# Kernel optimization log

Hardware: AMD Instinct MI355X
Metric: run time of the kernel (lower is better)

Reference implementation:

```python
import jax, jax.numpy as jnp
import numpy as np

ALPHA = 0.1  # LeakyReLU slope

def _leaky(v):
    return jnp.where(v >= 0, v, ALPHA * v)

def setup_inputs() -> dict:
    key = jax.random.key(0)
    k1, k2, k3 = jax.random.split(key, 3)
    B, D_IN, D1, D2 = 262144, 200, 150, 100
    x = jax.random.normal(k1, (B, D_IN), dtype=jnp.float32)
    W1 = jax.random.normal(k2, (D_IN, D1), dtype=jnp.float32) * 0.05
    b1 = jnp.zeros((D1,), dtype=jnp.float32)
    W2 = jax.random.normal(k3, (D1, D2), dtype=jnp.float32) * 0.05
    b2 = jnp.zeros((D2,), dtype=jnp.float32)
    return {"x": x, "W1": W1, "b1": b1, "W2": W2, "b2": b2}

def reference(x, W1, b1, W2, b2):
    # Original loops per sample: dense(200->150)+LeakyReLU, mean -> out1;
    # dense(150->100)+LeakyReLU, mean -> out2. Batched here as single GEMMs.
    h1 = _leaky(x @ W1 + b1)           # [B, 150]
    out1 = jnp.mean(h1, axis=-1)       # [B]
    h2 = _leaky(h1 @ W2 + b2)          # [B, 100]
    out2 = jnp.mean(h2, axis=-1)       # [B]
    return (out1, out2)
```

## Files before the change

### kernel.cpp

```cpp
#include <hip/hip_runtime.h>

typedef unsigned short u16;
typedef unsigned int u32;
typedef __bf16 bf16x8 __attribute__((ext_vector_type(8)));
typedef float f32x4 __attribute__((ext_vector_type(4)));

#define W2F_OFF 71680
#define B1_OFF 107520
#define B2_OFF 108160
#define WS_BYTES 108608

__device__ __align__(256) unsigned char g_wbuf[WS_BYTES];

__device__ __forceinline__ u16 f2bf(float f) {
  __bf16 b = (__bf16)f;
  return __builtin_bit_cast(u16, b);
}
__device__ __forceinline__ u32 pk2bf(float a, float b) {
  return (u32)f2bf(a) | ((u32)f2bf(b) << 16);
}

__global__ void prep_kernel(const float* __restrict__ W1, const float* __restrict__ b1,
                            const float* __restrict__ W2, const float* __restrict__ b2)
{
  const int stride = gridDim.x * blockDim.x;
  const int tid0 = blockIdx.x * blockDim.x + threadIdx.x;
  u16* w1f = (u16*)g_wbuf;
  for (int e = tid0; e < 35840; e += stride) {
    int j = e & 7, l = (e >> 3) & 63, nt = (e >> 9) % 10, kt = e / 5120;
    int k = kt * 32 + ((l >> 4) << 3) + j;
    int n = nt * 16 + (l & 15);
    w1f[e] = (k < 200 && n < 150) ? f2bf(W1[k * 150 + n]) : (u16)0;
  }
  u16* w2f = (u16*)(g_wbuf + W2F_OFF);
  for (int e = tid0; e < 17920; e += stride) {
    int j = e & 7, l = (e >> 3) & 63, nt = (e >> 9) % 7, kt = e / 3584;
    int k = kt * 32 + ((l >> 4) << 3) + j;
    int n = nt * 16 + (l & 15);
    w2f[e] = (k < 150 && n < 100) ? f2bf(W2[k * 100 + n]) : (u16)0;
  }
  float* b1p = (float*)(g_wbuf + B1_OFF);
  for (int e = tid0; e < 160; e += stride) b1p[e] = (e < 150) ? b1[e] : 0.f;
  float* b2p = (float*)(g_wbuf + B2_OFF);
  for (int e = tid0; e < 112; e += stride) b2p[e] = (e < 100) ? b2[e] : 0.f;
}

__global__ __launch_bounds__(512, 5)
void fused_mlp(const float* __restrict__ x, float* __restrict__ out, int B)
{
  __shared__ __align__(16) u16 xs[12800];
  __shared__ float ps[2][2][64];

  const int tid = threadIdx.x;
  const int lane = tid & 63;
  const int wv = tid >> 6;
  const int h = wv & 1;
  const int mt = wv >> 1;
  const int cl = lane & 15, gr = lane >> 4;
  const long r0 = (long)blockIdx.x * 64;

  const u16* w1g = (const u16*)g_wbuf;
  const u16* w2g = (const u16*)(g_wbuf + W2F_OFF);

  const float* xg = x + r0 * 200;
  #pragma unroll
  for (int i = 0; i < 7; ++i) {
    int c = tid + i * 512;
    if (c < 3200) {
      int row = c / 50, kc = c % 50;
      float4 v = *reinterpret_cast<const float4*>(xg + row * 200 + kc * 4);
      int k0 = kc * 4;
      int m = row >> 4;
      int idx;
      if (k0 < 192) {
        int F = m * 6 + (k0 >> 5);
        int fl = (row & 15) | (((k0 & 31) >> 3) << 4);
        idx = (F * 64 + (fl ^ (F & 7))) * 8 + (k0 & 7);
      } else {
        idx = 12288 + m * 128 + (row & 15) * 8 + (k0 - 192);
      }
      uint2 p;
      p.x = pk2bf(v.x, v.y);
      p.y = pk2bf(v.z, v.w);
      *reinterpret_cast<uint2*>(&xs[idx]) = p;
    }
  }

  bf16x8 bfr[5];
  #pragma unroll
  for (int nt = 0; nt < 5; ++nt)
    bfr[nt] = *reinterpret_cast<const bf16x8*>(w1g + ((0 * 10 + 5 * h + nt) * 64 + lane) * 8);

  __syncthreads();

  const f32x4 zz = {0.f, 0.f, 0.f, 0.f};
  f32x4 acc1[5];
  #pragma unroll
  for (int nt = 0; nt < 5; ++nt) acc1[nt] = zz;

  #pragma unroll
  for (int kt = 0; kt < 7; ++kt) {
    bf16x8 bnx[5];
    if (kt < 6) {
      #pragma unroll
      for (int nt = 0; nt < 5; ++nt)
        bnx[nt] = *reinterpret_cast<const bf16x8*>(w1g + (((kt + 1) * 10 + 5 * h + nt) * 64 + lane) * 8);
    }
    bf16x8 a;
    if (kt < 6) {
      int F = mt * 6 + kt;
      a = *reinterpret_cast<const bf16x8*>(&xs[(F * 64 + (lane ^ (F & 7))) * 8]);
    } else {
      union { bf16x8 v; u32 w[4]; } A;
      A.v = *reinterpret_cast<const bf16x8*>(&xs[12288 + mt * 128 + cl * 8]);
      if (gr != 0) { A.w[0] = A.w[1] = A.w[2] = A.w[3] = 0u; }
      a = A.v;
    }
    #pragma unroll
    for (int nt = 0; nt < 5; ++nt)
      acc1[nt] = __builtin_amdgcn_mfma_f32_16x16x32_bf16(a, bfr[nt], acc1[nt], 0, 0, 0);
    if (kt < 6) {
      #pragma unroll
      for (int nt = 0; nt < 5; ++nt) bfr[nt] = bnx[nt];
    }
  }
  __syncthreads();

  const float* b1p = (const float*)(g_wbuf + B1_OFF);
  float b1v[5];
  #pragma unroll
  for (int nt = 0; nt < 5; ++nt) b1v[nt] = b1p[(5 * h + nt) * 16 + cl];

  float rs[4] = {0, 0, 0, 0};
  #pragma unroll
  for (int nt = 0; nt < 5; ++nt) {
    int k2 = (5 * h + nt) * 16 + cl;
    int kt2 = k2 >> 5;
    int l2base = 16 * ((k2 & 31) >> 3);
    int e2 = k2 & 7;
    #pragma unroll
    for (int j = 0; j < 4; ++j) {
      int l2 = gr * 4 + j + l2base;
      float hv = acc1[nt][j] + b1v[nt];
      hv = (hv >= 0.f) ? hv : 0.1f * hv;
      rs[j] += hv;
      xs[((mt * 5 + kt2) * 64 + l2) * 8 + e2] = f2bf(hv);
    }
  }
  #pragma unroll
  for (int j = 0; j < 4; ++j) {
    float s = rs[j];
    #pragma unroll
    for (int mask = 1; mask < 16; mask <<= 1) s += __shfl_xor(s, mask, 64);
    if (cl == 0) ps[0][h][mt * 16 + gr * 4 + j] = s;
  }
  __syncthreads();

  if (tid < 64)
    out[r0 + tid] = (ps[0][0][tid] + ps[0][1][tid]) * (1.f / 150.f);

  f32x4 acc2[4];
  #pragma unroll
  for (int nt = 0; nt < 4; ++nt) acc2[nt] = zz;

  #pragma unroll
  for (int kt = 0; kt < 5; ++kt) {
    bf16x8 a = *reinterpret_cast<const bf16x8*>(&xs[((mt * 5 + kt) * 64 + lane) * 8]);
    #pragma unroll
    for (int nt = 0; nt < 4; ++nt) {
      if (nt < 3 || h == 0) {
        bf16x8 b = *reinterpret_cast<const bf16x8*>(w2g + ((kt * 7 + 4 * h + nt) * 64 + lane) * 8);
        acc2[nt] = __builtin_amdgcn_mfma_f32_16x16x32_bf16(a, b, acc2[nt], 0, 0, 0);
      }
    }
  }

  const float* b2p = (const float*)(g_wbuf + B2_OFF);
  float b2v[4];
  #pragma unroll
  for (int nt = 0; nt < 4; ++nt)
    b2v[nt] = (nt < 3 || h == 0) ? b2p[(4 * h + nt) * 16 + cl] : 0.f;

  float ts[4] = {0, 0, 0, 0};
  #pragma unroll
  for (int nt = 0; nt < 4; ++nt) {
    if (nt < 3 || h == 0) {
      #pragma unroll
      for (int j = 0; j < 4; ++j) {
        float hv = acc2[nt][j] + b2v[nt];
        hv = (hv >= 0.f) ? hv : 0.1f * hv;
        ts[j] += hv;
      }
    }
  }
  #pragma unroll
  for (int j = 0; j < 4; ++j) {
    float s = ts[j];
    #pragma unroll
    for (int mask = 1; mask < 16; mask <<= 1) s += __shfl_xor(s, mask, 64);
    if (cl == 0) ps[1][h][mt * 16 + gr * 4 + j] = s;
  }
  __syncthreads();

  if (tid < 64)
    out[B + r0 + tid] = (ps[1][0][tid] + ps[1][1][tid]) * (1.f / 100.f);
}

extern "C" void kernel_launch(void* const* d_in, const int* in_sizes, int n_in,
                              void* d_out, int out_size, void* d_ws, size_t ws_size,
                              hipStream_t stream)
{
  const float* x  = (const float*)d_in[0];
  const float* W1 = (const float*)d_in[1];
  const float* b1 = (const float*)d_in[2];
  const float* W2 = (const float*)d_in[3];
  const float* b2 = (const float*)d_in[4];
  float* out = (float*)d_out;
  const int B = in_sizes[0] / 200;

  prep_kernel<<<64, 256, 0, stream>>>(W1, b1, W2, b2);
  fused_mlp<<<B / 64, 512, 0, stream>>>(x, out, B);
}
```

Before: 85.27 us.

## Split work by output column tiles across 5 waves, each covering all 64 rows

Reorganizes the fused MLP block from 8 waves (4 row tiles x 2 column halves) to 5 waves, each owning 2 column tiles of layer 1 across all 4 row tiles. Each W1/W2 fragment is now loaded once per wave and reused over 4 MFMAs, which cuts redundant global weight fetches. Layer-2 weights are now prefetched one k-step ahead. In exchange there are fewer threads per block, more accumulator registers per wave and a 5-way partial-sum reduction, which may lower occupancy and slow the x load phase.

```diff
diff --git a/kernel.cpp b/kernel.cpp
--- a/kernel.cpp
+++ b/kernel.cpp
@@ -45,17 +45,15 @@
   for (int e = tid0; e < 112; e += stride) b2p[e] = (e < 100) ? b2[e] : 0.f;
 }
 
-__global__ __launch_bounds__(512, 5)
+__global__ __launch_bounds__(320, 4)
 void fused_mlp(const float* __restrict__ x, float* __restrict__ out, int B)
 {
   __shared__ __align__(16) u16 xs[12800];
-  __shared__ float ps[2][2][64];
+  __shared__ float ps[2][5][64];
 
   const int tid = threadIdx.x;
   const int lane = tid & 63;
   const int wv = tid >> 6;
-  const int h = wv & 1;
-  const int mt = wv >> 1;
   const int cl = lane & 15, gr = lane >> 4;
   const long r0 = (long)blockIdx.x * 64;
 
@@ -64,146 +62,192 @@
 
   const float* xg = x + r0 * 200;
   #pragma unroll
-  for (int i = 0; i < 7; ++i) {
-    int c = tid + i * 512;
-    if (c < 3200) {
-      int row = c / 50, kc = c % 50;
-      float4 v = *reinterpret_cast<const float4*>(xg + row * 200 + kc * 4);
-      int k0 = kc * 4;
-      int m = row >> 4;
-      int idx;
-      if (k0 < 192) {
-        int F = m * 6 + (k0 >> 5);
-        int fl = (row & 15) | (((k0 & 31) >> 3) << 4);
-        idx = (F * 64 + (fl ^ (F & 7))) * 8 + (k0 & 7);
-      } else {
-        idx = 12288 + m * 128 + (row & 15) * 8 + (k0 - 192);
-      }
-      uint2 p;
-      p.x = pk2bf(v.x, v.y);
-      p.y = pk2bf(v.z, v.w);
-      *reinterpret_cast<uint2*>(&xs[idx]) = p;
-    }
-  }
-
-  bf16x8 bfr[5];
-  #pragma unroll
-  for (int nt = 0; nt < 5; ++nt)
-    bfr[nt] = *reinterpret_cast<const bf16x8*>(w1g + ((0 * 10 + 5 * h + nt) * 64 + lane) * 8);
+  for (int i = 0; i < 10; ++i) {
+    int c = tid + i * 320;
+    int row = c / 50, kc = c % 50;
+    float4 v = *reinterpret_cast<const float4*>(xg + row * 200 + kc * 4);
+    int k0 = kc * 4;
+    int mt = row >> 4;
+    int idx;
+    if (k0 < 192) {
+      int F = mt * 6 + (k0 >> 5);
+      int fl = (row & 15) | (((k0 & 31) >> 3) << 4);
+      idx = (F * 64 + (fl ^ (F & 7))) * 8 + (k0 & 7);
+    } else {
+      idx = 12288 + mt * 128 + (row & 15) * 8 + (k0 - 192);
+    }
+    uint2 p;
+    p.x = pk2bf(v.x, v.y);
+    p.y = pk2bf(v.z, v.w);
+    *reinterpret_cast<uint2*>(&xs[idx]) = p;
+  }
+
+  bf16x8 bfr[2];
+  #pragma unroll
+  for (int nt = 0; nt < 2; ++nt)
+    bfr[nt] = *reinterpret_cast<const bf16x8*>(w1g + ((0 * 10 + 2 * wv + nt) * 64 + lane) * 8);
 
   __syncthreads();
 
   const f32x4 zz = {0.f, 0.f, 0.f, 0.f};
-  f32x4 acc1[5];
-  #pragma unroll
-  for (int nt = 0; nt < 5; ++nt) acc1[nt] = zz;
+  f32x4 acc1[2][4];
+  #pragma unroll
+  for (int nt = 0; nt < 2; ++nt)
+    #pragma unroll
+    for (int mt = 0; mt < 4; ++mt) acc1[nt][mt] = zz;
 
   #pragma unroll
   for (int kt = 0; kt < 7; ++kt) {
-    bf16x8 bnx[5];
+    bf16x8 bnx[2];
     if (kt < 6) {
       #pragma unroll
-      for (int nt = 0; nt < 5; ++nt)
-        bnx[nt] = *reinterpret_cast<const bf16x8*>(w1g + (((kt + 1) * 10 + 5 * h + nt) * 64 + lane) * 8);
-    }
-    bf16x8 a;
+      for (int nt = 0; nt < 2; ++nt)
+        bnx[nt] = *reinterpret_cast<const bf16x8*>(w1g + (((kt + 1) * 10 + 2 * wv + nt) * 64 + lane) * 8);
+    }
+    bf16x8 a[4];
     if (kt < 6) {
-      int F = mt * 6 + kt;
-      a = *reinterpret_cast<const bf16x8*>(&xs[(F * 64 + (lane ^ (F & 7))) * 8]);
+      #pragma unroll
+      for (int mt = 0; mt < 4; ++mt) {
+        int F = mt * 6 + kt;
+        a[mt] = *reinterpret_cast<const bf16x8*>(&xs[(F * 64 + (lane ^ (F & 7))) * 8]);
+      }
     } else {
-      union { bf16x8 v; u32 w[4]; } A;
-      A.v = *reinterpret_cast<const bf16x8*>(&xs[12288 + mt * 128 + cl * 8]);
-      if (gr != 0) { A.w[0] = A.w[1] = A.w[2] = A.w[3] = 0u; }
-      a = A.v;
-    }
-    #pragma unroll
-    for (int nt = 0; nt < 5; ++nt)
-      acc1[nt] = __builtin_amdgcn_mfma_f32_16x16x32_bf16(a, bfr[nt], acc1[nt], 0, 0, 0);
+      #pragma unroll
+      for (int mt = 0; mt < 4; ++mt) {
+        union { bf16x8 v; u32 w[4]; } A;
+        A.v = *reinterpret_cast<const bf16x8*>(&xs[12288 + mt * 128 + cl * 8]);
+        if (gr != 0) { A.w[0] = A.w[1] = A.w[2] = A.w[3] = 0u; }
+        a[mt] = A.v;
+      }
+    }
+    #pragma unroll
+    for (int nt = 0; nt < 2; ++nt)
+      #pragma unroll
+      for (int mt = 0; mt < 4; ++mt)
+        acc1[nt][mt] = __builtin_amdgcn_mfma_f32_16x16x32_bf16(a[mt], bfr[nt], acc1[nt][mt], 0, 0, 0);
     if (kt < 6) {
-      #pragma unroll
-      for (int nt = 0; nt < 5; ++nt) bfr[nt] = bnx[nt];
+      bfr[0] = bnx[0]; bfr[1] = bnx[1];
     }
   }
   __syncthreads();
 
   const float* b1p = (const float*)(g_wbuf + B1_OFF);
-  float b1v[5];
-  #pragma unroll
-  for (int nt = 0; nt < 5; ++nt) b1v[nt] = b1p[(5 * h + nt) * 16 + cl];
-
-  float rs[4] = {0, 0, 0, 0};
-  #pragma unroll
-  for (int nt = 0; nt < 5; ++nt) {
-    int k2 = (5 * h + nt) * 16 + cl;
+  float b1v[2];
+  #pragma unroll
+  for (int nt = 0; nt < 2; ++nt) b1v[nt] = b1p[(2 * wv + nt) * 16 + cl];
+
+  float rs[4][4] = {{0,0,0,0},{0,0,0,0},{0,0,0,0},{0,0,0,0}};
+  #pragma unroll
+  for (int nt = 0; nt < 2; ++nt) {
+    int k2 = (2 * wv + nt) * 16 + cl;
     int kt2 = k2 >> 5;
     int l2base = 16 * ((k2 & 31) >> 3);
     int e2 = k2 & 7;
     #pragma unroll
+    for (int mt = 0; mt < 4; ++mt) {
+      #pragma unroll
+      for (int j = 0; j < 4; ++j) {
+        int l2 = gr * 4 + j + l2base;
+        float hv = acc1[nt][mt][j] + b1v[nt];
+        hv = (hv >= 0.f) ? hv : 0.1f * hv;
+        rs[mt][j] += hv;
+        xs[((mt * 5 + kt2) * 64 + l2) * 8 + e2] = f2bf(hv);
+      }
+    }
+  }
+  #pragma unroll
+  for (int mt = 0; mt < 4; ++mt)
+    #pragma unroll
     for (int j = 0; j < 4; ++j) {
-      int l2 = gr * 4 + j + l2base;
-      float hv = acc1[nt][j] + b1v[nt];
-      hv = (hv >= 0.f) ? hv : 0.1f * hv;
-      rs[j] += hv;
-      xs[((mt * 5 + kt2) * 64 + l2) * 8 + e2] = f2bf(hv);
-    }
-  }
-  #pragma unroll
-  for (int j = 0; j < 4; ++j) {
-    float s = rs[j];
-    #pragma unroll
-    for (int mask = 1; mask < 16; mask <<= 1) s += __shfl_xor(s, mask, 64);
-    if (cl == 0) ps[0][h][mt * 16 + gr * 4 + j] = s;
-  }
+      float s = rs[mt][j];
+      #pragma unroll
+      for (int mask = 1; mask < 16; mask <<= 1) s += __shfl_xor(s, mask, 64);
+      if (cl == 0) ps[0][wv][mt * 16 + gr * 4 + j] = s;
+    }
+
+  const int n2 = (wv < 2) ? 2 : 1;
+  const int base2 = (wv < 2) ? 2 * wv : wv + 2;
+  bf16x8 b2r[2];
+  #pragma unroll
+  for (int nt = 0; nt < 2; ++nt)
+    if (nt < n2)
+      b2r[nt] = *reinterpret_cast<const bf16x8*>(w2g + ((0 * 7 + base2 + nt) * 64 + lane) * 8);
+
   __syncthreads();
 
   if (tid < 64)
-    out[r0 + tid] = (ps[0][0][tid] + ps[0][1][tid]) * (1.f / 150.f);
-
-  f32x4 acc2[4];
-  #pragma unroll
-  for (int nt = 0; nt < 4; ++nt) acc2[nt] = zz;
+    out[r0 + tid] = (ps[0][0][tid] + ps[0][1][tid] + ps[0][2][tid] +
+                     ps[0][3][tid] + ps[0][4][tid]) * (1.f / 150.f);
+
+  f32x4 acc2[2][4];
+  #pragma unroll
+  for (int nt = 0; nt < 2; ++nt)
+    #pragma unroll
+    for (int mt = 0; mt < 4; ++mt) acc2[nt][mt] = zz;
 
   #pragma unroll
   for (int kt = 0; kt < 5; ++kt) {
-    bf16x8 a = *reinterpret_cast<const bf16x8*>(&xs[((mt * 5 + kt) * 64 + lane) * 8]);
-    #pragma unroll
-    for (int nt = 0; nt < 4; ++nt) {
-      if (nt < 3 || h == 0) {
-        bf16x8 b = *reinterpret_cast<const bf16x8*>(w2g + ((kt * 7 + 4 * h + nt) * 64 + lane) * 8);
-        acc2[nt] = __builtin_amdgcn_mfma_f32_16x16x32_bf16(a, b, acc2[nt], 0, 0, 0);
-      }
+    bf16x8 bnx2[2];
+    if (kt < 4) {
+      #pragma unroll
+      for (int nt = 0; nt < 2; ++nt)
+        if (nt < n2)
+          bnx2[nt] = *reinterpret_cast<const bf16x8*>(w2g + (((kt + 1) * 7 + base2 + nt) * 64 + lane) * 8);
+    }
+    bf16x8 a[4];
+    #pragma unroll
+    for (int mt = 0; mt < 4; ++mt)
+      a[mt] = *reinterpret_cast<const bf16x8*>(&xs[((mt * 5 + kt) * 64 + lane) * 8]);
+    #pragma unroll
+    for (int nt = 0; nt < 2; ++nt) {
+      if (nt < n2) {
+        #pragma unroll
+        for (int mt = 0; mt < 4; ++mt)
+          acc2[nt][mt] = __builtin_amdgcn_mfma_f32_16x16x32_bf16(a[mt], b2r[nt], acc2[nt][mt], 0, 0, 0);
+      }
+    }
+    if (kt < 4) {
+      #pragma unroll
+      for (int nt = 0; nt < 2; ++nt)
+        if (nt < n2) b2r[nt] = bnx2[nt];
     }
   }
 
   const float* b2p = (const float*)(g_wbuf + B2_OFF);
-  float b2v[4];
-  #pragma unroll
-  for (int nt = 0; nt < 4; ++nt)
-    b2v[nt] = (nt < 3 || h == 0) ? b2p[(4 * h + nt) * 16 + cl] : 0.f;
-
-  float ts[4] = {0, 0, 0, 0};
-  #pragma unroll
-  for (int nt = 0; nt < 4; ++nt) {
-    if (nt < 3 || h == 0) {
-      #pragma unroll
-      for (int j = 0; j < 4; ++j) {
-        float hv = acc2[nt][j] + b2v[nt];
-        hv = (hv >= 0.f) ? hv : 0.1f * hv;
-        ts[j] += hv;
-      }
-    }
-  }
-  #pragma unroll
-  for (int j = 0; j < 4; ++j) {
-    float s = ts[j];
-    #pragma unroll
-    for (int mask = 1; mask < 16; mask <<= 1) s += __shfl_xor(s, mask, 64);
-    if (cl == 0) ps[1][h][mt * 16 + gr * 4 + j] = s;
-  }
+  float b2v[2];
+  #pragma unroll
+  for (int nt = 0; nt < 2; ++nt)
+    b2v[nt] = (nt < n2) ? b2p[(base2 + nt) * 16 + cl] : 0.f;
+
+  float ts[4][4] = {{0,0,0,0},{0,0,0,0},{0,0,0,0},{0,0,0,0}};
+  #pragma unroll
+  for (int nt = 0; nt < 2; ++nt) {
+    if (nt < n2) {
+      #pragma unroll
+      for (int mt = 0; mt < 4; ++mt) {
+        #pragma unroll
+        for (int j = 0; j < 4; ++j) {
+          float hv = acc2[nt][mt][j] + b2v[nt];
+          hv = (hv >= 0.f) ? hv : 0.1f * hv;
+          ts[mt][j] += hv;
+        }
+      }
+    }
+  }
+  #pragma unroll
+  for (int mt = 0; mt < 4; ++mt)
+    #pragma unroll
+    for (int j = 0; j < 4; ++j) {
+      float s = ts[mt][j];
+      #pragma unroll
+      for (int mask = 1; mask < 16; mask <<= 1) s += __shfl_xor(s, mask, 64);
+      if (cl == 0) ps[1][wv][mt * 16 + gr * 4 + j] = s;
+    }
   __syncthreads();
 
   if (tid < 64)
-    out[B + r0 + tid] = (ps[1][0][tid] + ps[1][1][tid]) * (1.f / 100.f);
+    out[B + r0 + tid] = (ps[1][0][tid] + ps[1][1][tid] + ps[1][2][tid] +
+                         ps[1][3][tid] + ps[1][4][tid]) * (1.f / 100.f);
 }
 
 extern "C" void kernel_launch(void* const* d_in, const int* in_sizes, int n_in,
@@ -219,5 +263,5 @@
   const int B = in_sizes[0] / 200;
 
   prep_kernel<<<64, 256, 0, stream>>>(W1, b1, W2, b2);
-  fused_mlp<<<B / 64, 512, 0, stream>>>(x, out, B);
-}
+  fused_mlp<<<B / 64, 320, 0, stream>>>(x, out, B);
+}
```

New measurement: 122.2 us. 43.3% more time.
